# Performance work log

Measured on AMD Instinct MI355X. Metric: run time of the kernel, lower is better.

The kernel has to match this reference:

```python
import jax, jax.numpy as jnp
import numpy as np

B, N, K, C_IN, OC = 16, 4096, 16, 64, 64
OC2 = OC // 2
LEAK = 0.2
EPS = 1e-12  # guards sqrt grad when a neighbor equals the center point


def _cbn(x, w, s, b):
    # 1x1 conv (channel-last) + folded eval-mode BatchNorm: (x @ w.T) * s + b
    return jnp.einsum('...i,oi->...o', x, w) * s + b


def _lrelu(x):
    return jax.nn.leaky_relu(x, LEAK)


def _gather(feat, idx):
    # feat [B,N,C], idx [B,N,k] -> [B,N,k,C]  (index_points)
    return jax.vmap(lambda f, i: f[i])(feat, idx)


def _attentive_pool(x_info, feat, idx, wq, sq, bq, wk, sk, bk, wv, sv, bv, w2, s2, b2):
    q = jax.nn.relu(_cbn(feat, wq, sq, bq))   # [B,N,C]
    kf = jax.nn.relu(_cbn(feat, wk, sk, bk))
    vf = jax.nn.relu(_cbn(feat, wv, sv, bv))
    Kn = _gather(kf, idx)                     # [B,N,k,C]
    W = x_info * (Kn - q[:, :, None, :])      # [B,N,k,C]
    Vn = _gather(vf, idx)
    a = jax.nn.softmax(W, axis=2)             # softmax over k neighbors
    out = jnp.sum(a * Vn, axis=2)             # [B,N,C]
    return _lrelu(_cbn(out, w2, s2, b2))


def _forward(x, feature, neighbor_index,
             mlp1_w, mlp1_s, mlp1_b, lse1_w, lse1_s, lse1_b,
             p1_wq, p1_sq, p1_bq, p1_wk, p1_sk, p1_bk, p1_wv, p1_sv, p1_bv, p1_w2, p1_s2, p1_b2,
             lse2_w, lse2_s, lse2_b,
             p2_wq, p2_sq, p2_bq, p2_wk, p2_sk, p2_bk, p2_wv, p2_sv, p2_bv, p2_w2, p2_s2, p2_b2,
             mlp2_w, mlp2_s, mlp2_b, res_w, res_s, res_b):
    idx = neighbor_index
    xt = jnp.transpose(x, (0, 2, 1))          # [B,N,3]
    ft = jnp.transpose(feature, (0, 2, 1))    # [B,N,C_IN]
    identity = ft
    f1 = _lrelu(_cbn(ft, mlp1_w, mlp1_s, mlp1_b))        # [B,N,OC2]
    knn_x = _gather(xt, idx)                             # [B,N,k,3]
    center = jnp.broadcast_to(xt[:, :, None, :], knn_x.shape)
    diff = knn_x - center
    dist = jnp.sqrt(jnp.sum(diff * diff, axis=-1, keepdims=True) + EPS)  # [B,N,k,1]
    x_info = jnp.concatenate([center, knn_x, diff, dist], axis=-1)       # [B,N,k,10]
    x_info = _lrelu(_cbn(x_info, lse1_w, lse1_s, lse1_b))                # [B,N,k,OC2]
    feat2 = _attentive_pool(x_info, f1, idx,
                            p1_wq, p1_sq, p1_bq, p1_wk, p1_sk, p1_bk,
                            p1_wv, p1_sv, p1_bv, p1_w2, p1_s2, p1_b2)    # [B,N,OC2]
    x_info2 = _lrelu(_cbn(x_info, lse2_w, lse2_s, lse2_b))               # [B,N,k,OC2]
    feat3 = _attentive_pool(x_info2, feat2, idx,
                            p2_wq, p2_sq, p2_bq, p2_wk, p2_sk, p2_bk,
                            p2_wv, p2_sv, p2_bv, p2_w2, p2_s2, p2_b2)    # [B,N,OC]
    out = _cbn(feat3, mlp2_w, mlp2_s, mlp2_b)            # [B,N,2*OC]
    res = _cbn(identity, res_w, res_s, res_b)            # [B,N,2*OC]
    out = _lrelu(out + res)
    return jnp.transpose(out, (0, 2, 1))                 # [B,2*OC,N]


def setup_inputs() -> dict:
    key = jax.random.key(0)
    it = iter(jax.random.split(key, 80))
    nxt = lambda: next(it)

    def w(*shape):
        return jax.random.normal(nxt(), shape, jnp.float32) * 0.1

    def bn(c):
        s = jax.random.uniform(nxt(), (c,), jnp.float32, 0.5, 1.5)
        b = jax.random.normal(nxt(), (c,), jnp.float32) * 0.1
        return s, b

    inp = {
        'x': jax.random.normal(nxt(), (B, 3, N), jnp.float32),
        'feature': jax.random.normal(nxt(), (B, C_IN, N), jnp.float32),
        'neighbor_index': jax.random.randint(nxt(), (B, N, K), 0, N, jnp.int32),
    }
    inp['mlp1_w'] = w(OC2, C_IN); inp['mlp1_s'], inp['mlp1_b'] = bn(OC2)
    inp['lse1_w'] = w(OC2, 10); inp['lse1_s'], inp['lse1_b'] = bn(OC2)
    for p, co in (('p1', OC2), ('p2', OC)):
        inp[p + '_wq'] = w(OC2, OC2); inp[p + '_sq'], inp[p + '_bq'] = bn(OC2)
        inp[p + '_wk'] = w(OC2, OC2); inp[p + '_sk'], inp[p + '_bk'] = bn(OC2)
        inp[p + '_wv'] = w(OC2, OC2); inp[p + '_sv'], inp[p + '_bv'] = bn(OC2)
        inp[p + '_w2'] = w(co, OC2); inp[p + '_s2'], inp[p + '_b2'] = bn(co)
    inp['lse2_w'] = w(OC2, OC2); inp['lse2_s'], inp['lse2_b'] = bn(OC2)
    inp['mlp2_w'] = w(2 * OC, OC); inp['mlp2_s'], inp['mlp2_b'] = bn(2 * OC)
    inp['res_w'] = w(2 * OC, C_IN); inp['res_s'], inp['res_b'] = bn(2 * OC)
    return inp


def reference(x, feature, neighbor_index,
              mlp1_w, mlp1_s, mlp1_b, lse1_w, lse1_s, lse1_b,
              p1_wq, p1_sq, p1_bq, p1_wk, p1_sk, p1_bk, p1_wv, p1_sv, p1_bv, p1_w2, p1_s2, p1_b2,
              lse2_w, lse2_s, lse2_b,
              p2_wq, p2_sq, p2_bq, p2_wk, p2_sk, p2_bk, p2_wv, p2_sv, p2_bv, p2_w2, p2_s2, p2_b2,
              mlp2_w, mlp2_s, mlp2_b, res_w, res_s, res_b):
    return _forward(x, feature, neighbor_index,
                    mlp1_w, mlp1_s, mlp1_b, lse1_w, lse1_s, lse1_b,
                    p1_wq, p1_sq, p1_bq, p1_wk, p1_sk, p1_bk, p1_wv, p1_sv, p1_bv, p1_w2, p1_s2, p1_b2,
                    lse2_w, lse2_s, lse2_b,
                    p2_wq, p2_sq, p2_bq, p2_wk, p2_sk, p2_bk, p2_wv, p2_sv, p2_bv, p2_w2, p2_s2, p2_b2,
                    mlp2_w, mlp2_s, mlp2_b, res_w, res_s, res_b)
```

## Files before the change

kernel.cpp:

```cpp
#include <hip/hip_runtime.h>
#include <cstdint>
#include <cstddef>

#define NB 16
#define NP 4096
#define KNN 16
#define CIN 64
#define H 32
#define OCC 64
#define PN ((size_t)NB*NP)

__device__ __forceinline__ float lrelu(float v){ return v > 0.f ? v : 0.2f*v; }
__device__ __forceinline__ float reluf(float v){ return v > 0.f ? v : 0.f; }

typedef __attribute__((ext_vector_type(8)))  short bf16x8s;
typedef __attribute__((ext_vector_type(4)))  float f32x4;
typedef __attribute__((ext_vector_type(16))) float f32x16;

__device__ __forceinline__ short f2bf(float f){
    union { float f; unsigned u; } v; v.f = f;
    unsigned r = v.u + 0x7fffu + ((v.u >> 16) & 1u);
    return (short)(r >> 16);
}

__global__ __launch_bounds__(256) void k_pointwise(
    const float* __restrict__ feat, const float* __restrict__ xpos,
    const float* __restrict__ w1, const float* __restrict__ s1, const float* __restrict__ b1,
    const float* __restrict__ wq, const float* __restrict__ sq, const float* __restrict__ bq,
    const float* __restrict__ wk, const float* __restrict__ sk, const float* __restrict__ bk,
    const float* __restrict__ wv, const float* __restrict__ sv, const float* __restrict__ bv,
    float* __restrict__ q1, float* __restrict__ kv1,
    float* __restrict__ xp, short* __restrict__ ftp,
    const float* __restrict__ m2w, const float* __restrict__ m2s, const float* __restrict__ m2b,
    const float* __restrict__ rw, const float* __restrict__ rs, const float* __restrict__ rb,
    const float* __restrict__ p2w2,
    short* __restrict__ wbigW, short* __restrict__ w2bW, float* __restrict__ bbW)
{
    __shared__ float ftile[CIN][65];
    __shared__ float f1t[H][65];
    int t = threadIdx.x;
    int l = t & 63;
    int g = __builtin_amdgcn_readfirstlane(t >> 6);
    int bid = blockIdx.x;
    int b  = bid >> 6;
    int n0 = (bid & 63) * 64;
    int n  = n0 + l;
    size_t p = (size_t)b*NP + n;

    const float* fb = feat + ((size_t)b*CIN)*NP + n;
    float fv[16];
    #pragma unroll
    for (int k=0;k<16;k++){
        int c = g*16 + k;
        fv[k] = fb[(size_t)c*NP];
        ftile[c][l] = fv[k];
    }
    {
        bf16x8s h0, h1;
        #pragma unroll
        for (int i=0;i<8;i++){ h0[i] = f2bf(fv[i]); h1[i] = f2bf(fv[8+i]); }
        *(bf16x8s*)(ftp + p*64 + g*16)     = h0;
        *(bf16x8s*)(ftp + p*64 + g*16 + 8) = h1;
    }
    if (g == 0){
        const float* xb = xpos + (size_t)b*3*NP;
        *(float4*)(xp + 4*p) = make_float4(xb[n], xb[NP+n], xb[2*NP+n], 0.f);
    }
    __syncthreads();

    float acc[8];
    #pragma unroll
    for (int u=0;u<8;u++) acc[u] = 0.f;
    #pragma unroll
    for (int c=0;c<CIN;c++){
        float x = ftile[c][l];
        #pragma unroll
        for (int u=0;u<8;u++) acc[u] = fmaf(w1[(g*8+u)*CIN+c], x, acc[u]);
    }
    #pragma unroll
    for (int u=0;u<8;u++){
        int h = g*8+u;
        f1t[h][l] = lrelu(acc[u]*s1[h] + b1[h]);
    }
    __syncthreads();

    float aq[8], ak[8], av[8];
    #pragma unroll
    for (int u=0;u<8;u++){ aq[u]=0.f; ak[u]=0.f; av[u]=0.f; }
    #pragma unroll
    for (int j=0;j<H;j++){
        float x = f1t[j][l];
        #pragma unroll
        for (int u=0;u<8;u++){
            int h = g*8+u;
            aq[u] = fmaf(wq[h*H+j], x, aq[u]);
            ak[u] = fmaf(wk[h*H+j], x, ak[u]);
            av[u] = fmaf(wv[h*H+j], x, av[u]);
        }
    }
    float qr[8], kr[8], vr[8];
    #pragma unroll
    for (int u=0;u<8;u++){
        int h = g*8+u;
        qr[u] = reluf(aq[u]*sq[h]+bq[h]);
        kr[u] = reluf(ak[u]*sk[h]+bk[h]);
        vr[u] = reluf(av[u]*sv[h]+bv[h]);
    }
    size_t qb = p*H + g*8;
    *(float4*)(q1+qb)   = make_float4(qr[0],qr[1],qr[2],qr[3]);
    *(float4*)(q1+qb+4) = make_float4(qr[4],qr[5],qr[6],qr[7]);
    size_t kb = (p*H + g*8)*2;
    #pragma unroll
    for (int u2=0;u2<4;u2++)
        *(float4*)(kv1+kb+u2*4) = make_float4(kr[u2*2],vr[u2*2],kr[u2*2+1],vr[u2*2+1]);

    if (bid == 0){
        int o = t >> 1, half = t & 1;
        const float* srcp = half ? (rw + (size_t)o*64) : (m2w + (size_t)o*64);
        float sc = half ? rs[o] : m2s[o];
        short* dst = wbigW + (size_t)o*128 + half*64;
        #pragma unroll
        for (int j=0;j<64;j+=8){
            bf16x8s v8;
            #pragma unroll
            for (int i=0;i<8;i++) v8[i] = f2bf(srcp[j+i]*sc);
            *(bf16x8s*)(dst + j) = v8;
        }
        if (!half) bbW[o] = m2b[o] + rb[o];
        {
            int i0 = t*8;
            bf16x8s w8;
            #pragma unroll
            for (int i=0;i<8;i++) w8[i] = f2bf(p2w2[i0+i]);
            *(bf16x8s*)(w2bW + i0) = w8;
        }
    }
}

__global__ __launch_bounds__(256) void k_pool1(
    const float* __restrict__ xp, const int* __restrict__ nidx,
    const float* __restrict__ q1, const float* __restrict__ kv1,
    const float* __restrict__ l1w, const float* __restrict__ l1s, const float* __restrict__ l1b,
    const float* __restrict__ w2, const float* __restrict__ s2, const float* __restrict__ b2,
    const float* __restrict__ wq, const float* __restrict__ sq, const float* __restrict__ bq,
    const float* __restrict__ wk, const float* __restrict__ sk, const float* __restrict__ bk,
    const float* __restrict__ wv, const float* __restrict__ sv, const float* __restrict__ bv,
    float* __restrict__ q2, float* __restrict__ kv2)
{
    __shared__ float wl[4][32*36];
    __shared__ float bcp[4][2][32];
    __shared__ float bcf[4][2][32];
    int t = threadIdx.x;
    {
        const float* wsrc[4] = {w2, wq, wk, wv};
        #pragma unroll
        for (int m=0;m<4;m++)
            for (int i=t;i<1024;i+=256)
                wl[m][(i>>5)*36 + (i&31)] = wsrc[m][i];
    }
    __syncthreads();

    int wv_ = t >> 6;
    int l   = t & 63;
    int n_  = l & 31;
    int hi  = l >> 5;
    int bid = blockIdx.x;
    int sb  = ((bid & 7) << 10) | (bid >> 3);
    size_t p0 = (size_t)sb*8 + (size_t)wv_*2;
    int b = (int)(p0 >> 12);

    bf16x8s Bf;
    if (hi == 0){
        #pragma unroll
        for (int i=0;i<8;i++) Bf[i] = f2bf(l1w[n_*10 + i]);
    } else {
        Bf[0] = f2bf(l1w[n_*10 + 8]);
        Bf[1] = f2bf(l1w[n_*10 + 9]);
        #pragma unroll
        for (int i=2;i<8;i++) Bf[i] = 0;
    }

    int ptA  = (l >> 4) & 1;
    int nbrA = l & 15;
    size_t pA = p0 + ptA;
    int idA = nidx[pA*KNN + nbrA];
    float4 cp = *(const float4*)(xp + 4*pA);
    float4 nv = *(const float4*)(xp + 4*((size_t)(b<<12)+idA));
    float dx = nv.x-cp.x, dy = nv.y-cp.y, dz = nv.z-cp.z;
    float dist = sqrtf(dx*dx+dy*dy+dz*dz + 1e-12f);
    bf16x8s A;
    if (hi == 0){
        A[0]=f2bf(cp.x); A[1]=f2bf(cp.y); A[2]=f2bf(cp.z); A[3]=f2bf(nv.x);
        A[4]=f2bf(nv.y); A[5]=f2bf(nv.z); A[6]=f2bf(dx);   A[7]=f2bf(dy);
    } else {
        A[0]=f2bf(dz); A[1]=f2bf(dist);
        A[2]=0; A[3]=0; A[4]=0; A[5]=0; A[6]=0; A[7]=0;
    }

    f32x16 cz = {0.f,0.f,0.f,0.f,0.f,0.f,0.f,0.f,0.f,0.f,0.f,0.f,0.f,0.f,0.f,0.f};
    f32x16 D = __builtin_amdgcn_mfma_f32_32x32x16_bf16(A, Bf, cz, 0, 0, 0);

    float sl1 = l1s[n_], bl1 = l1b[n_];
    const int* irow0 = nidx + p0*KNN;
    float outv[2];
    #pragma unroll
    for (int pt=0; pt<2; pt++){
        size_t p = p0 + pt;
        float qc = q1[p*H + n_];
        int4 idlo = *(const int4*)(irow0 + pt*KNN + 4*hi);
        int4 idhi = *(const int4*)(irow0 + pt*KNN + 8 + 4*hi);
        int ids[8] = {idlo.x,idlo.y,idlo.z,idlo.w, idhi.x,idhi.y,idhi.z,idhi.w};
        float W[8], V[8];
        #pragma unroll
        for (int rr=0; rr<8; rr++){
            float xi = lrelu(D[pt*8+rr]*sl1 + bl1);
            float2 kv = *(const float2*)(kv1 + 2*(((size_t)b*NP + ids[rr])*H + n_));
            W[rr] = xi*(kv.x - qc);
            V[rr] = kv.y;
        }
        float mx = W[0];
        #pragma unroll
        for (int rr=1;rr<8;rr++) mx = fmaxf(mx, W[rr]);
        mx = fmaxf(mx, __shfl_xor(mx, 32, 64));
        float den = 0.f, ac = 0.f;
        #pragma unroll
        for (int rr=0;rr<8;rr++){
            float e = __expf(W[rr]-mx);
            den += e; ac = fmaf(e, V[rr], ac);
        }
        den += __shfl_xor(den, 32, 64);
        ac  += __shfl_xor(ac,  32, 64);
        outv[pt] = ac/den;
    }
    if (l < 32){ bcp[wv_][0][n_] = outv[0]; bcp[wv_][1][n_] = outv[1]; }

    int c = n_;
    float f2a = 0.f;
    #pragma unroll
    for (int jj=0;jj<8;jj++){
        float4 xv = *(const float4*)&bcp[wv_][hi][jj*4];
        float4 w4 = *(const float4*)&wl[0][c*36 + jj*4];
        f2a += w4.x*xv.x + w4.y*xv.y + w4.z*xv.z + w4.w*xv.w;
    }
    float f2 = lrelu(f2a*s2[c] + b2[c]);
    bcf[wv_][hi][c] = f2;

    float aq=0.f, ak=0.f, av=0.f;
    #pragma unroll
    for (int jj=0;jj<8;jj++){
        float4 xv  = *(const float4*)&bcf[wv_][hi][jj*4];
        float4 wq4 = *(const float4*)&wl[1][c*36 + jj*4];
        float4 wk4 = *(const float4*)&wl[2][c*36 + jj*4];
        float4 wv4 = *(const float4*)&wl[3][c*36 + jj*4];
        aq += wq4.x*xv.x + wq4.y*xv.y + wq4.z*xv.z + wq4.w*xv.w;
        ak += wk4.x*xv.x + wk4.y*xv.y + wk4.z*xv.z + wk4.w*xv.w;
        av += wv4.x*xv.x + wv4.y*xv.y + wv4.z*xv.z + wv4.w*xv.w;
    }
    size_t base = (p0 + hi)*H + c;
    q2[base] = reluf(aq*sq[c]+bq[c]);
    *(float2*)(kv2 + 2*base) = make_float2(reluf(ak*sk[c]+bk[c]), reluf(av*sv[c]+bv[c]));
}

__global__ __launch_bounds__(512) void k_pool2(
    const float* __restrict__ xp, const int* __restrict__ nidx,
    const float* __restrict__ q2, const float* __restrict__ kv2,
    const float* __restrict__ l1w, const float* __restrict__ l1s, const float* __restrict__ l1b,
    const float* __restrict__ l2w, const float* __restrict__ l2s, const float* __restrict__ l2b,
    const short* __restrict__ w2bf, const float* __restrict__ s2, const float* __restrict__ b2,
    const short* __restrict__ ftp, const short* __restrict__ wbig, const float* __restrict__ bb,
    float* __restrict__ out)
{
    __shared__ unsigned short xiT[8][32*40];
    __shared__ unsigned short bcb[16][40];
    __shared__ unsigned short xf[16][72];
    int t = threadIdx.x;
    int wv_ = t >> 6;
    int l   = t & 63;
    int n_  = l & 31;
    int hi  = l >> 5;
    int bid = blockIdx.x;
    int sb  = ((bid & 7) << 9) | (bid >> 3);
    size_t pbase = (size_t)sb * 16;
    size_t p0 = pbase + (size_t)wv_*2;
    int b = (int)(pbase >> 12);

    bf16x8s Bf1;
    if (hi == 0){
        #pragma unroll
        for (int i=0;i<8;i++) Bf1[i] = f2bf(l1w[n_*10 + i]);
    } else {
        Bf1[0] = f2bf(l1w[n_*10 + 8]);
        Bf1[1] = f2bf(l1w[n_*10 + 9]);
        #pragma unroll
        for (int i=2;i<8;i++) Bf1[i] = 0;
    }
    int ptA  = (l >> 4) & 1;
    int nbrA = l & 15;
    size_t pA = p0 + ptA;
    int idA = nidx[pA*KNN + nbrA];
    float4 cp = *(const float4*)(xp + 4*pA);
    float4 nv = *(const float4*)(xp + 4*((size_t)(b<<12)+idA));
    float dx = nv.x-cp.x, dy = nv.y-cp.y, dz = nv.z-cp.z;
    float dist = sqrtf(dx*dx+dy*dy+dz*dz + 1e-12f);
    bf16x8s Ag;
    if (hi == 0){
        Ag[0]=f2bf(cp.x); Ag[1]=f2bf(cp.y); Ag[2]=f2bf(cp.z); Ag[3]=f2bf(nv.x);
        Ag[4]=f2bf(nv.y); Ag[5]=f2bf(nv.z); Ag[6]=f2bf(dx);   Ag[7]=f2bf(dy);
    } else {
        Ag[0]=f2bf(dz); Ag[1]=f2bf(dist);
        Ag[2]=0; Ag[3]=0; Ag[4]=0; Ag[5]=0; Ag[6]=0; Ag[7]=0;
    }
    f32x16 cz = {0.f,0.f,0.f,0.f,0.f,0.f,0.f,0.f,0.f,0.f,0.f,0.f,0.f,0.f,0.f,0.f};
    f32x16 D1 = __builtin_amdgcn_mfma_f32_32x32x16_bf16(Ag, Bf1, cz, 0, 0, 0);

    float sl1 = l1s[n_], bl1 = l1b[n_];
    #pragma unroll
    for (int r=0;r<16;r++){
        int m = (r&3) + 8*(r>>2) + 4*hi;
        xiT[wv_][m*40 + n_] = (unsigned short)f2bf(lrelu(D1[r]*sl1 + bl1));
    }
    bf16x8s A20 = *(const bf16x8s*)&xiT[wv_][n_*40 + hi*8];
    bf16x8s A21 = *(const bf16x8s*)&xiT[wv_][n_*40 + 16 + hi*8];
    bf16x8s B0, B1;
    {
        const float* r0 = l2w + n_*32 + hi*8;
        #pragma unroll
        for (int i=0;i<8;i++){ B0[i] = f2bf(r0[i]); B1[i] = f2bf(r0[16+i]); }
    }
    f32x16 D = __builtin_amdgcn_mfma_f32_32x32x16_bf16(A20, B0, cz, 0, 0, 0);
    D = __builtin_amdgcn_mfma_f32_32x32x16_bf16(A21, B1, D, 0, 0, 0);

    float sl2 = l2s[n_], bl2 = l2b[n_];
    const int* irow0 = nidx + p0*KNN;
    float outv[2];
    #pragma unroll
    for (int pt=0; pt<2; pt++){
        size_t p = p0 + pt;
        float qc = q2[p*H + n_];
        int4 idlo = *(const int4*)(irow0 + pt*KNN + 4*hi);
        int4 idhi = *(const int4*)(irow0 + pt*KNN + 8 + 4*hi);
        int ids[8] = {idlo.x,idlo.y,idlo.z,idlo.w, idhi.x,idhi.y,idhi.z,idhi.w};
        float W[8], V[8];
        #pragma unroll
        for (int rr=0; rr<8; rr++){
            float xi2 = lrelu(D[pt*8+rr]*sl2 + bl2);
            float2 kv = *(const float2*)(kv2 + 2*(((size_t)b*NP + ids[rr])*H + n_));
            W[rr] = xi2*(kv.x - qc);
            V[rr] = kv.y;
        }
        float mx = W[0];
        #pragma unroll
        for (int rr=1;rr<8;rr++) mx = fmaxf(mx, W[rr]);
        mx = fmaxf(mx, __shfl_xor(mx, 32, 64));
        float den = 0.f, ac = 0.f;
        #pragma unroll
        for (int rr=0;rr<8;rr++){
            float e = __expf(W[rr]-mx);
            den += e; ac = fmaf(e, V[rr], ac);
        }
        den += __shfl_xor(den, 32, 64);
        ac  += __shfl_xor(ac,  32, 64);
        outv[pt] = ac/den;
    }
    if (l < 32){
        bcb[wv_*2 + 0][n_] = (unsigned short)f2bf(outv[0]);
        bcb[wv_*2 + 1][n_] = (unsigned short)f2bf(outv[1]);
    }
    __syncthreads();

    int lr = l & 15, kg = l >> 4;
    if (wv_ < 4){
        bf16x8s Aw = *(const bf16x8s*)(w2bf + (wv_*16 + lr)*32 + kg*8);
        bf16x8s Bp = *(const bf16x8s*)&bcb[lr][kg*8];
        f32x4 zz = {0.f,0.f,0.f,0.f};
        f32x4 Df = __builtin_amdgcn_mfma_f32_16x16x32_bf16(Aw, Bp, zz, 0, 0, 0);
        int ch0 = wv_*16 + kg*4;
        float4 s4 = *(const float4*)(s2 + ch0);
        float4 b4 = *(const float4*)(b2 + ch0);
        xf[lr][ch0+0] = (unsigned short)f2bf(lrelu(Df[0]*s4.x + b4.x));
        xf[lr][ch0+1] = (unsigned short)f2bf(lrelu(Df[1]*s4.y + b4.y));
        xf[lr][ch0+2] = (unsigned short)f2bf(lrelu(Df[2]*s4.z + b4.z));
        xf[lr][ch0+3] = (unsigned short)f2bf(lrelu(Df[3]*s4.w + b4.w));
    }
    __syncthreads();

    int o0 = wv_ * 16;
    const short* wr = wbig + (size_t)(o0 + lr)*128 + kg*8;
    bf16x8s Af0 = *(const bf16x8s*)(wr);
    bf16x8s Af1 = *(const bf16x8s*)(wr + 32);
    bf16x8s Af2 = *(const bf16x8s*)(wr + 64);
    bf16x8s Af3 = *(const bf16x8s*)(wr + 96);
    bf16x8s Bx0 = *(const bf16x8s*)&xf[lr][kg*8];
    bf16x8s Bx1 = *(const bf16x8s*)&xf[lr][32 + kg*8];
    const short* fr = ftp + (pbase + lr)*64 + kg*8;
    bf16x8s Bx2 = *(const bf16x8s*)(fr);
    bf16x8s Bx3 = *(const bf16x8s*)(fr + 32);
    f32x4 Dq = {0.f,0.f,0.f,0.f};
    Dq = __builtin_amdgcn_mfma_f32_16x16x32_bf16(Af0, Bx0, Dq, 0, 0, 0);
    Dq = __builtin_amdgcn_mfma_f32_16x16x32_bf16(Af1, Bx1, Dq, 0, 0, 0);
    Dq = __builtin_amdgcn_mfma_f32_16x16x32_bf16(Af2, Bx2, Dq, 0, 0, 0);
    Dq = __builtin_amdgcn_mfma_f32_16x16x32_bf16(Af3, Bx3, Dq, 0, 0, 0);
    float4 bb4 = *(const float4*)(bb + o0 + kg*4);
    int n0 = (int)(pbase & (NP-1));
    float* ob = out + ((size_t)b*128)*NP + n0 + lr;
    ob[(size_t)(o0 + kg*4 + 0)*NP] = lrelu(Dq[0] + bb4.x);
    ob[(size_t)(o0 + kg*4 + 1)*NP] = lrelu(Dq[1] + bb4.y);
    ob[(size_t)(o0 + kg*4 + 2)*NP] = lrelu(Dq[2] + bb4.z);
    ob[(size_t)(o0 + kg*4 + 3)*NP] = lrelu(Dq[3] + bb4.w);
}

extern "C" void kernel_launch(void* const* d_in, const int* in_sizes, int n_in,
                              void* d_out, int out_size, void* d_ws, size_t ws_size,
                              hipStream_t stream)
{
    (void)in_sizes; (void)n_in; (void)out_size; (void)ws_size;
    const float* x     = (const float*)d_in[0];
    const float* feat  = (const float*)d_in[1];
    const int*   nidx  = (const int*)  d_in[2];
    const float* m1w=(const float*)d_in[3],  *m1s=(const float*)d_in[4],  *m1b=(const float*)d_in[5];
    const float* l1w=(const float*)d_in[6],  *l1s=(const float*)d_in[7],  *l1b=(const float*)d_in[8];
    const float* p1wq=(const float*)d_in[9],  *p1sq=(const float*)d_in[10], *p1bq=(const float*)d_in[11];
    const float* p1wk=(const float*)d_in[12], *p1sk=(const float*)d_in[13], *p1bk=(const float*)d_in[14];
    const float* p1wv=(const float*)d_in[15], *p1sv=(const float*)d_in[16], *p1bv=(const float*)d_in[17];
    const float* p1w2=(const float*)d_in[18], *p1s2=(const float*)d_in[19], *p1b2=(const float*)d_in[20];
    const float* p2wq=(const float*)d_in[21], *p2sq=(const float*)d_in[22], *p2bq=(const float*)d_in[23];
    const float* p2wk=(const float*)d_in[24], *p2sk=(const float*)d_in[25], *p2bk=(const float*)d_in[26];
    const float* p2wv=(const float*)d_in[27], *p2sv=(const float*)d_in[28], *p2bv=(const float*)d_in[29];
    const float* p2w2=(const float*)d_in[30], *p2s2=(const float*)d_in[31], *p2b2=(const float*)d_in[32];
    const float* l2w=(const float*)d_in[33], *l2s=(const float*)d_in[34], *l2b=(const float*)d_in[35];
    const float* m2w=(const float*)d_in[36], *m2s=(const float*)d_in[37], *m2b=(const float*)d_in[38];
    const float* rw =(const float*)d_in[39], *rs =(const float*)d_in[40], *rb =(const float*)d_in[41];

    float* ws = (float*)d_ws;
    float* q1  = ws;
    float* kv1 = ws + PN*32;
    float* q2  = ws + PN*96;
    float* kv2 = ws + PN*128;
    float* xp  = ws + PN*192;
    short* ftp = (short*)(ws + PN*196);
    short* wbig = (short*)(ws + PN*228);
    short* w2bf = wbig + 16384;
    float* bb   = (float*)(w2bf + 2048);

    float* outp = (float*)d_out;

    k_pointwise<<<dim3(PN/64),dim3(256),0,stream>>>(feat, x, m1w,m1s,m1b,
        p1wq,p1sq,p1bq, p1wk,p1sk,p1bk, p1wv,p1sv,p1bv, q1,kv1, xp, ftp,
        m2w,m2s,m2b, rw,rs,rb, p2w2, wbig, w2bf, bb);
    k_pool1<<<dim3(PN/8),dim3(256),0,stream>>>(xp,nidx, q1,kv1,
        l1w,l1s,l1b, p1w2,p1s2,p1b2,
        p2wq,p2sq,p2bq, p2wk,p2sk,p2bk, p2wv,p2sv,p2bv, q2,kv2);
    k_pool2<<<dim3(PN/16),dim3(512),0,stream>>>(xp,nidx, q2,kv2,
        l1w,l1s,l1b, l2w,l2s,l2b, w2bf, p2s2, p2b2, ftp, wbig, bb, outp);
}
```

Measured before the change: 301.9 us.

## Compute pointwise mlp1 and q/k/v projections with bf16 MFMA instructions

Replaces the scalar FMA loops in the pointwise kernel with 16x16x32 bf16 MFMA ops. Features are staged as bf16 in shared memory, and weights are scaled by the BN factor and converted to bf16 per lane. The mlp1 output is kept in shared memory as bf16 before the q/k/v projections. This cuts ALU work in the first stage but lowers precision of the intermediate f1 and the q/k/v outputs to bf16 inputs.

```diff
diff --git a/kernel.cpp b/kernel.cpp
--- a/kernel.cpp
+++ b/kernel.cpp
@@ -36,84 +36,34 @@
     const float* __restrict__ p2w2,
     short* __restrict__ wbigW, short* __restrict__ w2bW, float* __restrict__ bbW)
 {
-    __shared__ float ftile[CIN][65];
-    __shared__ float f1t[H][65];
+    __shared__ unsigned short ftb[64*72];
+    __shared__ unsigned short f1b[64*40];
     int t = threadIdx.x;
     int l = t & 63;
-    int g = __builtin_amdgcn_readfirstlane(t >> 6);
+    int g = t >> 6;
     int bid = blockIdx.x;
     int b  = bid >> 6;
     int n0 = (bid & 63) * 64;
     int n  = n0 + l;
     size_t p = (size_t)b*NP + n;
 
-    const float* fb = feat + ((size_t)b*CIN)*NP + n;
-    float fv[16];
-    #pragma unroll
-    for (int k=0;k<16;k++){
-        int c = g*16 + k;
-        fv[k] = fb[(size_t)c*NP];
-        ftile[c][l] = fv[k];
-    }
-    {
+    {
+        const float* fb = feat + ((size_t)b*CIN)*NP + n;
+        float fv[16];
+        #pragma unroll
+        for (int k=0;k<16;k++) fv[k] = fb[(size_t)(g*16+k)*NP];
         bf16x8s h0, h1;
         #pragma unroll
         for (int i=0;i<8;i++){ h0[i] = f2bf(fv[i]); h1[i] = f2bf(fv[8+i]); }
         *(bf16x8s*)(ftp + p*64 + g*16)     = h0;
         *(bf16x8s*)(ftp + p*64 + g*16 + 8) = h1;
+        *(bf16x8s*)&ftb[l*72 + g*16]       = h0;
+        *(bf16x8s*)&ftb[l*72 + g*16 + 8]   = h1;
     }
     if (g == 0){
         const float* xb = xpos + (size_t)b*3*NP;
         *(float4*)(xp + 4*p) = make_float4(xb[n], xb[NP+n], xb[2*NP+n], 0.f);
     }
-    __syncthreads();
-
-    float acc[8];
-    #pragma unroll
-    for (int u=0;u<8;u++) acc[u] = 0.f;
-    #pragma unroll
-    for (int c=0;c<CIN;c++){
-        float x = ftile[c][l];
-        #pragma unroll
-        for (int u=0;u<8;u++) acc[u] = fmaf(w1[(g*8+u)*CIN+c], x, acc[u]);
-    }
-    #pragma unroll
-    for (int u=0;u<8;u++){
-        int h = g*8+u;
-        f1t[h][l] = lrelu(acc[u]*s1[h] + b1[h]);
-    }
-    __syncthreads();
-
-    float aq[8], ak[8], av[8];
-    #pragma unroll
-    for (int u=0;u<8;u++){ aq[u]=0.f; ak[u]=0.f; av[u]=0.f; }
-    #pragma unroll
-    for (int j=0;j<H;j++){
-        float x = f1t[j][l];
-        #pragma unroll
-        for (int u=0;u<8;u++){
-            int h = g*8+u;
-            aq[u] = fmaf(wq[h*H+j], x, aq[u]);
-            ak[u] = fmaf(wk[h*H+j], x, ak[u]);
-            av[u] = fmaf(wv[h*H+j], x, av[u]);
-        }
-    }
-    float qr[8], kr[8], vr[8];
-    #pragma unroll
-    for (int u=0;u<8;u++){
-        int h = g*8+u;
-        qr[u] = reluf(aq[u]*sq[h]+bq[h]);
-        kr[u] = reluf(ak[u]*sk[h]+bk[h]);
-        vr[u] = reluf(av[u]*sv[h]+bv[h]);
-    }
-    size_t qb = p*H + g*8;
-    *(float4*)(q1+qb)   = make_float4(qr[0],qr[1],qr[2],qr[3]);
-    *(float4*)(q1+qb+4) = make_float4(qr[4],qr[5],qr[6],qr[7]);
-    size_t kb = (p*H + g*8)*2;
-    #pragma unroll
-    for (int u2=0;u2<4;u2++)
-        *(float4*)(kv1+kb+u2*4) = make_float4(kr[u2*2],vr[u2*2],kr[u2*2+1],vr[u2*2+1]);
-
     if (bid == 0){
         int o = t >> 1, half = t & 1;
         const float* srcp = half ? (rw + (size_t)o*64) : (m2w + (size_t)o*64);
@@ -134,6 +84,93 @@
             for (int i=0;i<8;i++) w8[i] = f2bf(p2w2[i0+i]);
             *(bf16x8s*)(w2bW + i0) = w8;
         }
+    }
+    __syncthreads();
+
+    int lr = t & 15;
+    int kg = (t >> 4) & 3;
+    int prow = g*16 + lr;
+    size_t pg = (size_t)b*NP + n0 + prow;
+
+    f32x4 Df0 = {0.f,0.f,0.f,0.f}, Df1 = {0.f,0.f,0.f,0.f};
+    #pragma unroll
+    for (int kk=0; kk<2; kk++){
+        bf16x8s Bf = *(const bf16x8s*)&ftb[prow*72 + kk*32 + kg*8];
+        {
+            int h = lr;
+            float sc = s1[h];
+            const float* wr = w1 + h*64 + kk*32 + kg*8;
+            bf16x8s Aw;
+            #pragma unroll
+            for (int i=0;i<8;i++) Aw[i] = f2bf(wr[i]*sc);
+            Df0 = __builtin_amdgcn_mfma_f32_16x16x32_bf16(Aw, Bf, Df0, 0, 0, 0);
+        }
+        {
+            int h = 16 + lr;
+            float sc = s1[h];
+            const float* wr = w1 + h*64 + kk*32 + kg*8;
+            bf16x8s Aw;
+            #pragma unroll
+            for (int i=0;i<8;i++) Aw[i] = f2bf(wr[i]*sc);
+            Df1 = __builtin_amdgcn_mfma_f32_16x16x32_bf16(Aw, Bf, Df1, 0, 0, 0);
+        }
+    }
+    {
+        int ch = kg*4;
+        float4 b4 = *(const float4*)(b1 + ch);
+        unsigned u0 = (unsigned short)f2bf(lrelu(Df0[0]+b4.x))
+                    | ((unsigned)(unsigned short)f2bf(lrelu(Df0[1]+b4.y)) << 16);
+        unsigned u1 = (unsigned short)f2bf(lrelu(Df0[2]+b4.z))
+                    | ((unsigned)(unsigned short)f2bf(lrelu(Df0[3]+b4.w)) << 16);
+        *(uint2*)&f1b[prow*40 + ch] = make_uint2(u0, u1);
+    }
+    {
+        int ch = 16 + kg*4;
+        float4 b4 = *(const float4*)(b1 + ch);
+        unsigned u0 = (unsigned short)f2bf(lrelu(Df1[0]+b4.x))
+                    | ((unsigned)(unsigned short)f2bf(lrelu(Df1[1]+b4.y)) << 16);
+        unsigned u1 = (unsigned short)f2bf(lrelu(Df1[2]+b4.z))
+                    | ((unsigned)(unsigned short)f2bf(lrelu(Df1[3]+b4.w)) << 16);
+        *(uint2*)&f1b[prow*40 + ch] = make_uint2(u0, u1);
+    }
+
+    bf16x8s Bq = *(const bf16x8s*)&f1b[prow*40 + kg*8];
+    float qv[6][4];
+    {
+        const float* wsrc[3] = {wq, wk, wv};
+        const float* ssrc[3] = {sq, sk, sv};
+        const float* bsrc[3] = {bq, bk, bv};
+        #pragma unroll
+        for (int m3=0; m3<3; m3++){
+            #pragma unroll
+            for (int mt=0; mt<2; mt++){
+                int h = mt*16 + lr;
+                float sc = ssrc[m3][h];
+                const float* wr = wsrc[m3] + h*32 + kg*8;
+                bf16x8s Aw;
+                #pragma unroll
+                for (int i=0;i<8;i++) Aw[i] = f2bf(wr[i]*sc);
+                f32x4 Dq = {0.f,0.f,0.f,0.f};
+                Dq = __builtin_amdgcn_mfma_f32_16x16x32_bf16(Aw, Bq, Dq, 0, 0, 0);
+                int ch = mt*16 + kg*4;
+                float4 b4 = *(const float4*)(bsrc[m3] + ch);
+                qv[m3*2+mt][0] = reluf(Dq[0] + b4.x);
+                qv[m3*2+mt][1] = reluf(Dq[1] + b4.y);
+                qv[m3*2+mt][2] = reluf(Dq[2] + b4.z);
+                qv[m3*2+mt][3] = reluf(Dq[3] + b4.w);
+            }
+        }
+    }
+    size_t qb = pg*H;
+    *(float4*)(q1 + qb + kg*4)      = make_float4(qv[0][0],qv[0][1],qv[0][2],qv[0][3]);
+    *(float4*)(q1 + qb + 16 + kg*4) = make_float4(qv[1][0],qv[1][1],qv[1][2],qv[1][3]);
+    #pragma unroll
+    for (int mt=0; mt<2; mt++){
+        int ch = mt*16 + kg*4;
+        *(float4*)(kv1 + 2*(qb+ch))     = make_float4(qv[2+mt][0], qv[4+mt][0],
+                                                      qv[2+mt][1], qv[4+mt][1]);
+        *(float4*)(kv1 + 2*(qb+ch) + 4) = make_float4(qv[2+mt][2], qv[4+mt][2],
+                                                      qv[2+mt][3], qv[4+mt][3]);
     }
 }
 
```

Measured after the change: 294.6 us. -2.4%, faster.
